# Kernel optimization log

Measured on AMD Instinct MI355X. Metric: run time of the kernel, lower is better.

## Reference

```python
import jax, jax.numpy as jnp
import numpy as np

D = 256
H_GRID = 256
W_GRID = 256
N_LAYERS = 6


def _build_edges(H, W):
    # Vectorized equivalent of grid_to_graph's 4-neighbor edge construction.
    ii, jj = np.meshgrid(np.arange(H), np.arange(W), indexing='ij')
    srcs, dsts, feats = [], [], []
    for di, dj in [(-1, 0), (1, 0), (0, -1), (0, 1)]:
        ni, nj = ii + di, jj + dj
        m = (ni >= 0) & (ni < H) & (nj >= 0) & (nj < W)
        s = (ii * W + jj)[m]
        d = (ni * W + nj)[m]
        f = np.stack([
            np.full(s.shape, di, np.float32),
            np.full(s.shape, dj, np.float32),
            (ii[m] / H).astype(np.float32),
            (jj[m] / W).astype(np.float32),
        ], axis=-1)
        srcs.append(s); dsts.append(d); feats.append(f)
    edge_index = np.stack([np.concatenate(srcs), np.concatenate(dsts)]).astype(np.int32)
    edge_feats = np.concatenate(feats).astype(np.float32)
    return edge_index, edge_feats


def setup_inputs() -> dict:
    key = jax.random.key(0)
    ks = jax.random.split(key, 16)
    grid = jax.random.randint(ks[0], (H_GRID, W_GRID), 0, 10, dtype=jnp.int32)
    edge_index_np, edge_feats_np = _build_edges(H_GRID, W_GRID)
    edge_index = jnp.asarray(edge_index_np)
    edge_feats = jnp.asarray(edge_feats_np)

    def lin(k, fan_in, fan_out):
        bound = 1.0 / np.sqrt(fan_in)
        k1, k2 = jax.random.split(k)
        W = jax.random.uniform(k1, (fan_in, fan_out), jnp.float32, -bound, bound)
        b = jax.random.uniform(k2, (fan_out,), jnp.float32, -bound, bound)
        return W, b

    node_W, node_b = lin(ks[1], 1, D)

    def stack_lin(k, fan_in, fan_out):
        keys = jax.random.split(k, N_LAYERS)
        Ws, bs = zip(*[lin(kk, fan_in, fan_out) for kk in keys])
        return jnp.stack(Ws), jnp.stack(bs)

    msg_W1, msg_b1 = stack_lin(ks[2], 2 * D + 4, D)
    msg_W2, msg_b2 = stack_lin(ks[3], D, D)
    upd_W1, upd_b1 = stack_lin(ks[4], 2 * D, D)
    upd_W2, upd_b2 = stack_lin(ks[5], D, D)
    out_W, out_b = lin(ks[6], D, 10)

    return {
        'grid': grid, 'edge_index': edge_index, 'edge_feats': edge_feats,
        'node_W': node_W, 'node_b': node_b,
        'msg_W1': msg_W1, 'msg_b1': msg_b1, 'msg_W2': msg_W2, 'msg_b2': msg_b2,
        'upd_W1': upd_W1, 'upd_b1': upd_b1, 'upd_W2': upd_W2, 'upd_b2': upd_b2,
        'out_W': out_W, 'out_b': out_b,
    }


def reference(grid, edge_index, edge_feats, node_W, node_b,
              msg_W1, msg_b1, msg_W2, msg_b2,
              upd_W1, upd_b1, upd_W2, upd_b2,
              out_W, out_b):
    H, W = grid.shape
    N = H * W
    nodes = grid.astype(jnp.float32).reshape(N, 1)         # [N,1]
    h = nodes @ node_W + node_b                              # [N,D]
    src, tgt = edge_index[0], edge_index[1]

    def layer(h, params):
        mW1, mb1, mW2, mb2, uW1, ub1, uW2, ub2 = params
        # gather per-edge source/target features, run message MLP
        msg_in = jnp.concatenate([h[src], h[tgt], edge_feats], axis=-1)  # [E,2D+4]
        m = jax.nn.relu(msg_in @ mW1 + mb1) @ mW2 + mb2                   # [E,D]
        # scatter-add messages onto target nodes (vectorized segment sum)
        agg = jax.ops.segment_sum(m, tgt, num_segments=N)                 # [N,D]
        u_in = jnp.concatenate([h, agg], axis=-1)                         # [N,2D]
        h_new = jax.nn.relu(u_in @ uW1 + ub1) @ uW2 + ub2                 # [N,D]
        return h_new, None

    h, _ = jax.lax.scan(layer, h, (msg_W1, msg_b1, msg_W2, msg_b2,
                                   upd_W1, upd_b1, upd_W2, upd_b2))
    out = h @ out_W + out_b                                  # [N,10]
    return out.reshape(H, W, 10)
```

## Files before the change

### kernel.cpp

```cpp
#include <hip/hip_runtime.h>

#define HG 256
#define WGD 256
#define NN (HG*WGD)
#define NL 6

typedef _Float16 f16;
typedef _Float16 f16x8 __attribute__((ext_vector_type(8)));
typedef float f32x4 __attribute__((ext_vector_type(4)));

__device__ __forceinline__ void gload_lds16(const f16* g, f16* lds) {
  __builtin_amdgcn_global_load_lds(
      (const __attribute__((address_space(1))) unsigned int*)g,
      (__attribute__((address_space(3))) unsigned int*)lds, 16, 0, 0);
}

template<int KK, int EPI>
__global__ __launch_bounds__(512) void gemm8(
    const f16* __restrict__ A, int lda,
    const f16* __restrict__ Bt, int ldb,
    f16* __restrict__ C, int ldc,
    const float* __restrict__ bias,
    const float* __restrict__ v2,
    const float* __restrict__ avec,
    const int* __restrict__ gridv)
{
  constexpr int NT = KK/64;
  __shared__ f16 As[2][128*64];
  __shared__ f16 Bs[2][256*64];
  const int tid  = threadIdx.x;
  const int lane = tid & 63;
  const int w    = tid >> 6;
  const int wm   = w >> 2, wn = w & 3;

  int bid = blockIdx.x * gridDim.y + blockIdx.y;
  const int nwg = gridDim.x * gridDim.y;
  { int q = nwg >> 3; bid = (bid & 7) * q + (bid >> 3); }
  const int by = bid % gridDim.y, bx = bid / gridDim.y;
  const int mbase = bx * 128;
  const int nbase = by * 256;

  f32x4 acc[4][4];
#pragma unroll
  for (int a=0;a<4;a++)
#pragma unroll
    for (int b=0;b<4;b++) acc[a][b] = (f32x4){0.f,0.f,0.f,0.f};

  const int r8  = lane >> 3;
  const int c8s = ((lane & 7) ^ r8) * 8;

#define STAGE8(kt, buf)                                                        \
  {                                                                            \
    const f16* Ab = A + (size_t)mbase*lda + (kt)*64;                           \
    _Pragma("unroll")                                                          \
    for (int p=0;p<2;p++) {                                                    \
      int qc = p*8 + w;                                                        \
      gload_lds16(Ab + (size_t)(qc*8 + r8)*lda + c8s, &As[buf][qc*512]);       \
    }                                                                          \
    const f16* Bb = Bt + (size_t)nbase*ldb + (kt)*64;                          \
    _Pragma("unroll")                                                          \
    for (int p=0;p<4;p++) {                                                    \
      int qc = p*8 + w;                                                        \
      gload_lds16(Bb + (size_t)(qc*8 + r8)*ldb + c8s, &Bs[buf][qc*512]);       \
    }                                                                          \
  }

  STAGE8(0, 0);
  __syncthreads();
  int cur = 0;
  for (int kt = 0; kt < NT; ++kt) {
    if (kt + 1 < NT) STAGE8(kt + 1, cur ^ 1);
    const f16* Acur = &As[cur][0];
    const f16* Bcur = &Bs[cur][0];
#pragma unroll
    for (int ks=0; ks<2; ++ks) {
      const int off = (((ks*4 + (lane>>4)) ^ (lane & 7)) * 8);
      f16x8 af[4], bf[4];
#pragma unroll
      for (int fm=0; fm<4; ++fm)
        af[fm] = *(const f16x8*)&Acur[(wm*64 + fm*16 + (lane&15))*64 + off];
#pragma unroll
      for (int fn=0; fn<4; ++fn)
        bf[fn] = *(const f16x8*)&Bcur[(wn*64 + fn*16 + (lane&15))*64 + off];
#pragma unroll
      for (int fm=0; fm<4; ++fm)
#pragma unroll
        for (int fn=0; fn<4; ++fn)
          acc[fm][fn] = __builtin_amdgcn_mfma_f32_16x16x32_f16(af[fm], bf[fn], acc[fm][fn], 0,0,0);
    }
    __syncthreads();
    cur ^= 1;
  }
#undef STAGE8

  const int row0 = mbase + wm*64 + (lane>>4)*4;
  const int col0 = nbase + wn*64 + (lane&15);
#pragma unroll
  for (int fm=0; fm<4; ++fm) {
#pragma unroll
    for (int fn=0; fn<4; ++fn) {
      const int col = col0 + fn*16;
#pragma unroll
      for (int r=0;r<4;r++) {
        int row = row0 + fm*16 + r;
        float v = acc[fm][fn][r];
        if (EPI==1 || EPI==3) {
          int i = row >> 8, j = row & 255;
          float deg = (float)((i>0)+(i<255)+(j>0)+(j<255));
          v += bias[col & 255] + deg * v2[col & 255];
          if (EPI==3) v += (float)gridv[row] * avec[col & 255];
          v = fmaxf(v, 0.f);
        } else if (EPI==2) {
          v += bias[col];
        }
        C[(size_t)row*ldc + col] = (f16)v;
      }
    }
  }
}

__device__ __forceinline__ void gemm_core256(
    const f16* __restrict__ A, int lda,
    const f16* __restrict__ Bt, int ldb,
    f16* __restrict__ C, int ldc,
    int mbase, int nbase, f16* As, f16* Bs)
{
  const int tid  = threadIdx.x;
  const int lane = tid & 63;
  const int w    = tid >> 6;
  const int wm   = w >> 1, wn = w & 1;

  f32x4 acc[4][4];
#pragma unroll
  for (int a=0;a<4;a++)
#pragma unroll
    for (int b=0;b<4;b++) acc[a][b] = (f32x4){0.f,0.f,0.f,0.f};

  const int r8  = lane >> 3;
  const int c8s = ((lane & 7) ^ r8) * 8;

  for (int kt = 0; kt < 4; ++kt) {
    const f16* Ab = A  + (size_t)(mbase + w*32)*lda + kt*64;
    const f16* Bb = Bt + (size_t)(nbase + w*32)*ldb + kt*64;
#pragma unroll
    for (int i=0;i<4;i++) {
      gload_lds16(Ab + (size_t)(i*8 + r8)*lda + c8s, &As[(w*32+i*8)*64]);
      gload_lds16(Bb + (size_t)(i*8 + r8)*ldb + c8s, &Bs[(w*32+i*8)*64]);
    }
    __syncthreads();
#pragma unroll
    for (int ks=0; ks<2; ++ks) {
      const int off = (((ks*4 + (lane>>4)) ^ (lane & 7)) * 8);
      f16x8 af[4], bf[4];
#pragma unroll
      for (int fm=0; fm<4; ++fm)
        af[fm] = *(const f16x8*)&As[(wm*64 + fm*16 + (lane&15))*64 + off];
#pragma unroll
      for (int fn=0; fn<4; ++fn)
        bf[fn] = *(const f16x8*)&Bs[(wn*64 + fn*16 + (lane&15))*64 + off];
#pragma unroll
      for (int fm=0; fm<4; ++fm)
#pragma unroll
        for (int fn=0; fn<4; ++fn)
          acc[fm][fn] = __builtin_amdgcn_mfma_f32_16x16x32_f16(af[fm], bf[fn], acc[fm][fn], 0,0,0);
    }
    __syncthreads();
  }

  const int row0 = mbase + wm*64 + (lane>>4)*4;
  const int col0 = nbase + wn*64 + (lane&15);
#pragma unroll
  for (int fm=0; fm<4; ++fm)
#pragma unroll
    for (int fn=0; fn<4; ++fn)
#pragma unroll
      for (int r=0;r<4;r++)
        C[(size_t)(row0 + fm*16 + r)*ldc + (col0 + fn*16)] = (f16)acc[fm][fn][r];
}

__global__ __launch_bounds__(256) void fold_all(
    const f16* __restrict__ BtA,  const f16* __restrict__ uW2h,
    const f16* __restrict__ mW2h, const f16* __restrict__ uW1aT,
    const f16* __restrict__ uW1bT,const f16* __restrict__ oWTh,
    f16* __restrict__ BtPQ, f16* __restrict__ BtU, f16* __restrict__ Wp2t)
{
  __shared__ f16 As[128*64];
  __shared__ f16 Bs[128*64];
  const int b = blockIdx.x;
  if (b < 40) {
    int z = b >> 3, rem = b & 7, x = rem & 3, y = rem >> 2;
    gemm_core256(BtA + (size_t)(z+1)*131072, 256, uW2h + (size_t)z*65536, 256,
                 BtPQ + (size_t)(z+1)*131072, 256, x*128, y*128, As, Bs);
  } else if (b < 60) {
    int rem = b - 40, z = rem >> 2, r2 = rem & 3, x = r2 & 1, y = r2 >> 1;
    gemm_core256(uW1aT + (size_t)(z+1)*65536, 256, uW2h + (size_t)z*65536, 256,
                 BtU + (size_t)(z+1)*131072, 512, x*128, y*128, As, Bs);
  } else if (b < 84) {
    int rem = b - 60, z = rem >> 2, r2 = rem & 3, x = r2 & 1, y = r2 >> 1;
    gemm_core256(uW1bT + (size_t)z*65536, 256, mW2h + (size_t)z*65536, 256,
                 BtU + (size_t)z*131072 + 256, 512, x*128, y*128, As, Bs);
  } else {
    int y = b - 84;
    gemm_core256(oWTh, 256, uW2h + (size_t)5*65536, 256,
                 Wp2t, 256, 0, y*128, As, Bs);
  }
}

template<int R1>
__global__ __launch_bounds__(256) void edge_fuse(
    const f16* __restrict__ PQ, f16* __restrict__ UR,
    const float* __restrict__ cvec, const float* __restrict__ wsi_,
    const float* __restrict__ wsj_,
    const int* __restrict__ gridv, const float* __restrict__ pa,
    const float* __restrict__ pc)
{
  const int t  = threadIdx.x;
  const int ln = t >> 5, ch = t & 31;
  int bid = blockIdx.x;
  bid = (bid & 7) * 1024 + (bid >> 3);
  const int n  = bid*8 + ln;
  const int i  = n >> 8, j = n & 255;
  const int co = ch*8;

  float q[8], pa0[8], pc0[8];
  if (R1) {
    float g = (float)gridv[n];
#pragma unroll
    for (int e=0;e<8;e++) {
      pa0[e] = pa[co+e]; pc0[e] = pc[co+e];
      q[e] = g*pa[256+co+e] + pc[256+co+e];
    }
  } else {
    f16x8 qv = *(const f16x8*)&PQ[(size_t)n*512 + 256 + co];
#pragma unroll
    for (int e=0;e<8;e++) q[e] = (float)qv[e];
  }
  float wi[8], wj[8];
#pragma unroll
  for (int e=0;e<8;e++){ wi[e]=wsi_[co+e]; wj[e]=wsj_[co+e]; }
  float acc[8];
#pragma unroll
  for (int e=0;e<8;e++) acc[e]=0.f;

  const int DI[4] = {-1,1,0,0};
  const int DJ[4] = {0,0,-1,1};
#pragma unroll
  for (int d=0; d<4; ++d) {
    int si = i - DI[d], sj = j - DJ[d];
    if (si>=0 && si<HG && sj>=0 && sj<WGD) {
      int s = si*WGD + sj;
      float fsi = si * (1.f/HG), fsj = sj * (1.f/WGD);
      float pvf[8];
      if (R1) {
        float gs = (float)gridv[s];
#pragma unroll
        for (int e=0;e<8;e++) pvf[e] = gs*pa0[e] + pc0[e];
      } else {
        f16x8 pv = *(const f16x8*)&PQ[(size_t)s*512 + co];
#pragma unroll
        for (int e=0;e<8;e++) pvf[e] = (float)pv[e];
      }
#pragma unroll
      for (int e=0;e<8;e++) {
        float v = pvf[e] + q[e] + cvec[d*256+co+e] + fsi*wi[e] + fsj*wj[e];
        acc[e] += fmaxf(v, 0.f);
      }
    }
  }
  f16x8 outv;
#pragma unroll
  for (int e=0;e<8;e++) outv[e] = (f16)acc[e];
  *(f16x8*)&UR[(size_t)n*512 + 256 + co] = outv;
}

__global__ __launch_bounds__(256) void out_mfma(
    const f16* __restrict__ U,
    const f16* __restrict__ Wp2t,
    const float* __restrict__ ob2,
    float* __restrict__ out)
{
  int lane = threadIdx.x & 63;
  int wv   = threadIdx.x >> 6;
  int nbase = blockIdx.x*64 + wv*16;
  f32x4 acc = (f32x4){0.f,0.f,0.f,0.f};
  int r  = lane & 15;
  int kg = (lane >> 4) * 8;
  const f16* Up = U + (size_t)(nbase + r)*512 + kg;
  const f16* Bp = Wp2t + r*256 + kg;
#pragma unroll
  for (int kt=0; kt<8; ++kt) {
    f16x8 af = *(const f16x8*)(Up + kt*32);
    f16x8 bf = *(const f16x8*)(Bp + kt*32);
    acc = __builtin_amdgcn_mfma_f32_16x16x32_f16(af, bf, acc, 0,0,0);
  }
  int col = lane & 15;
  int row0 = (lane>>4)*4;
  if (col < 10) {
    float bo = ob2[col];
#pragma unroll
    for (int rr=0; rr<4; ++rr)
      out[(size_t)(nbase + row0 + rr)*10 + col] = acc[rr] + bo;
  }
}

__global__ __launch_bounds__(256) void prep_small(
    const float* __restrict__ uW2, const float* __restrict__ mW2,
    const float* __restrict__ oW,  const float* __restrict__ mW1,
    const float* __restrict__ mb1, const float* __restrict__ mb2,
    const float* __restrict__ uW1, const float* __restrict__ ub1,
    const float* __restrict__ ub2, const float* __restrict__ nb,
    const float* __restrict__ nW,  const float* __restrict__ ob,
    f16* __restrict__ uW2h, f16* __restrict__ mW2h, f16* __restrict__ oWTh,
    float* __restrict__ cvec, float* __restrict__ wsi_, float* __restrict__ wsj_,
    float* __restrict__ v2, float* __restrict__ ubias, float* __restrict__ avec,
    float* __restrict__ pqb, float* __restrict__ pa, float* __restrict__ pc,
    float* __restrict__ ob2,
    f16* __restrict__ BtA, f16* __restrict__ uW1aT, f16* __restrict__ uW1bT)
{
  __shared__ float red[3][4][64];
  __shared__ float tbuf[32][33];
  const int b = blockIdx.x;
  const int tid = threadIdx.x;
  if (b < 1536) {
    int idx = b*256 + tid;
    uW2h[idx] = (f16)uW2[idx];
    mW2h[idx] = (f16)mW2[idx];
  } else if (b < 1664) {
    int c = b - 1536, j = tid;
    oWTh[c*256 + j] = (c < 10) ? (f16)oW[j*10 + c] : (f16)0.f;
  } else if (b < 1670) {
    int l = b - 1664, j = tid;
    const float* base = mW1 + (size_t)l*516*256;
    float w512 = base[512*256 + j], w513 = base[513*256 + j];
    float b1 = mb1[l*256 + j];
    const int DI[4] = {-1,1,0,0};
    const int DJ[4] = {0,0,-1,1};
    for (int d=0;d<4;d++)
      cvec[(l*4+d)*256 + j] = (float)DI[d]*w512 + (float)DJ[d]*w513 + b1;
    wsi_[l*256+j] = base[514*256 + j];
    wsj_[l*256+j] = base[515*256 + j];
  } else if (b < 1694) {
    int pr = tid & 63, q = tid >> 6;
    int pair = (b-1670)*64 + pr;
    int l = pair >> 8, j = pair & 255;
    const float* prevb = l ? (ub2 + (l-1)*256) : nb;
    float s1=0.f, s2=0.f, s3=0.f;
    for (int t = q*64; t < q*64+64; ++t) {
      s1 += mb2[l*256+t] * uW1[((size_t)l*512+256+t)*256 + j];
      s2 += prevb[t]     * uW1[((size_t)l*512+t)*256 + j];
      if (l==0) s3 += nW[t] * uW1[(size_t)t*256 + j];
    }
    red[0][q][pr]=s1; red[1][q][pr]=s2; red[2][q][pr]=s3;
    __syncthreads();
    if (q==0) {
      float a = red[0][0][pr]+red[0][1][pr]+red[0][2][pr]+red[0][3][pr];
      float bb = red[1][0][pr]+red[1][1][pr]+red[1][2][pr]+red[1][3][pr];
      v2[pair] = a;
      ubias[pair] = ub1[pair] + bb;
      if (l==0) avec[j] = red[2][0][pr]+red[2][1][pr]+red[2][2][pr]+red[2][3][pr];
    }
  } else if (b < 1742) {
    int pr = tid & 63, q = tid >> 6;
    int pair = (b-1694)*64 + pr;
    int l = pair >> 9, c = pair & 511;
    int rowoff = (c < 256) ? 0 : 256;
    int cc = c & 255;
    const float* base = mW1 + (size_t)l*516*256 + (size_t)rowoff*256 + cc;
    float s1=0.f, s2=0.f;
    if (l==0) {
      for (int j=q*64; j<q*64+64; ++j) { float wv = base[(size_t)j*256]; s1 += nW[j]*wv; s2 += nb[j]*wv; }
    } else {
      const float* pb = ub2 + (l-1)*256;
      for (int j=q*64; j<q*64+64; ++j) s1 += pb[j]*base[(size_t)j*256];
    }
    red[0][q][pr]=s1; red[1][q][pr]=s2;
    __syncthreads();
    if (q==0) {
      float a = red[0][0][pr]+red[0][1][pr]+red[0][2][pr]+red[0][3][pr];
      if (l==0) { pa[c]=a; pc[c]=red[1][0][pr]+red[1][1][pr]+red[1][2][pr]+red[1][3][pr]; }
      else pqb[pair] = a;
    }
  } else if (b == 1742) {
    int c = tid >> 4, jg = tid & 15;
    float s = 0.f;
    if (c < 10)
      for (int j=jg*16; j<jg*16+16; ++j) s += ub2[5*256+j]*oW[j*10+c];
    red[0][c>>2][(c&3)*16+jg] = s;
    __syncthreads();
    if (jg==0 && c < 16) {
      float a=0.f;
      for (int t2=0;t2<16;t2++) a += red[0][c>>2][(c&3)*16+t2];
      ob2[c] = (c < 10) ? a + ob[c] : 0.f;
    }
  } else {
    int t = b - 1743;
    int z = t >> 6, rem = t & 63;
    int bxs = (rem & 7) * 32, bys = (rem >> 3) * 32;
    const int q = z / 6, l = z % 6;
    const float* s;
    f16* d;
    if (q == 0)      { s = mW1 + (size_t)l*516*256;          d = BtA   + (size_t)l*131072; }
    else if (q == 1) { s = mW1 + (size_t)l*516*256 + 65536;  d = BtA   + (size_t)l*131072 + 65536; }
    else if (q == 2) { s = uW1 + (size_t)l*131072;           d = uW1aT + (size_t)l*65536; }
    else             { s = uW1 + (size_t)l*131072 + 65536;   d = uW1bT + (size_t)l*65536; }
    const int tx = tid & 31, ty = tid >> 5;
#pragma unroll
    for (int rr=0; rr<4; ++rr)
      tbuf[ty+rr*8][tx] = s[(size_t)(bys+ty+rr*8)*256 + bxs+tx];
    __syncthreads();
#pragma unroll
    for (int rr=0; rr<4; ++rr)
      d[(size_t)(bxs+ty+rr*8)*256 + bys+tx] = (f16)tbuf[tx][ty+rr*8];
  }
}

extern "C" void kernel_launch(void* const* d_in, const int* in_sizes, int n_in,
                              void* d_out, int out_size, void* d_ws, size_t ws_size,
                              hipStream_t stream)
{
  const int*   gridv = (const int*) d_in[0];
  const float* nW   = (const float*)d_in[3];
  const float* nb   = (const float*)d_in[4];
  const float* mW1  = (const float*)d_in[5];
  const float* mb1  = (const float*)d_in[6];
  const float* mW2  = (const float*)d_in[7];
  const float* mb2  = (const float*)d_in[8];
  const float* uW1  = (const float*)d_in[9];
  const float* ub1  = (const float*)d_in[10];
  const float* uW2  = (const float*)d_in[11];
  const float* ub2  = (const float*)d_in[12];
  const float* oW   = (const float*)d_in[13];
  const float* ob   = (const float*)d_in[14];
  float* out = (float*)d_out;

  char* ws = (char*)d_ws;
  size_t off = 0;
  f16* URa  = (f16*)(ws + off); off += (size_t)NN*512*2;
  f16* URb  = (f16*)(ws + off); off += (size_t)NN*512*2;
  f16* BtA  = (f16*)(ws + off); off += 6*512*256*2;
  f16* BtPQ = (f16*)(ws + off); off += 6*512*256*2;
  f16* BtU  = (f16*)(ws + off); off += 6*256*512*2;
  f16* uW2h = (f16*)(ws + off); off += 6*256*256*2;
  f16* mW2h = (f16*)(ws + off); off += 6*256*256*2;
  f16* uW1aT= (f16*)(ws + off); off += 6*256*256*2;
  f16* uW1bT= (f16*)(ws + off); off += 6*256*256*2;
  f16* oWTh = (f16*)(ws + off); off += 128*256*2;
  f16* Wp2t = (f16*)(ws + off); off += 128*256*2;
  float* cvec = (float*)(ws + off); off += 6*4*256*4;
  float* wsi_ = (float*)(ws + off); off += 6*256*4;
  float* wsj_ = (float*)(ws + off); off += 6*256*4;
  float* v2   = (float*)(ws + off); off += 6*256*4;
  float* ubias= (float*)(ws + off); off += 6*256*4;
  float* pqb  = (float*)(ws + off); off += 6*512*4;
  float* pa   = (float*)(ws + off); off += 512*4;
  float* pc   = (float*)(ws + off); off += 512*4;
  float* avec = (float*)(ws + off); off += 256*4;
  float* ob2  = (float*)(ws + off); off += 16*4;

  prep_small<<<3279,256,0,stream>>>(uW2, mW2, oW, mW1, mb1, mb2, uW1, ub1, ub2,
                                    nb, nW, ob,
                                    uW2h, mW2h, oWTh, cvec, wsi_, wsj_,
                                    v2, ubias, avec, pqb, pa, pc, ob2,
                                    BtA, uW1aT, uW1bT);
  fold_all<<<86,256,0,stream>>>(BtA, uW2h, mW2h, uW1aT, uW1bT, oWTh,
                                BtPQ, BtU, Wp2t);

  edge_fuse<1><<<8192,256,0,stream>>>(nullptr, URa, cvec, wsi_, wsj_, gridv, pa, pc);
  gemm8<256,3><<<dim3(512,1),512,0,stream>>>(
      URa + 256, 512, BtU + 256, 512, URa, 512,
      ubias, v2, avec, gridv);

  f16* cur = URa; f16* nxt = URb;
  for (int l=1;l<NL;l++){
    gemm8<256,2><<<dim3(512,2),512,0,stream>>>(
        cur, 512, BtPQ + (size_t)l*131072, 256, nxt, 512,
        pqb + l*512, nullptr, nullptr, nullptr);
    edge_fuse<0><<<8192,256,0,stream>>>(nxt, cur, cvec + l*1024, wsi_ + l*256, wsj_ + l*256,
                                        nullptr, nullptr, nullptr);
    gemm8<512,1><<<dim3(512,1),512,0,stream>>>(
        cur, 512, BtU + (size_t)l*131072, 512, nxt, 512,
        ubias + l*256, v2 + l*256, nullptr, nullptr);
    f16* t = cur; cur = nxt; nxt = t;
  }

  out_mfma<<<1024,256,0,stream>>>(cur, Wp2t, ob2, out);
}
```

Before: 522.5 us.

## Fuse update GEMM with next layer's PQ projection GEMM per row tile

Adds a gemm_merge kernel that computes the update MLP output for a 128-row tile, stages the fp16 result in LDS, then immediately multiplies it by the next layer's PQ projection weights. This removes one kernel launch per layer and the global round-trip that re-read h to compute PQ. It needs an extra NN x 512 PQ buffer. The layer loop is restructured so the last layer still uses the plain gemm8.

```diff
diff --git a/kernel.cpp b/kernel.cpp
--- a/kernel.cpp
+++ b/kernel.cpp
@@ -114,6 +114,163 @@
           v += bias[col];
         }
         C[(size_t)row*ldc + col] = (f16)v;
+      }
+    }
+  }
+}
+
+template<int KK, int EPI>
+__global__ __launch_bounds__(512) void gemm_merge(
+    const f16* __restrict__ A, int lda,
+    const f16* __restrict__ BtU_,
+    const f16* __restrict__ BtPQ_,
+    f16* __restrict__ Uo,
+    f16* __restrict__ PQo,
+    const float* __restrict__ bias,
+    const float* __restrict__ v2,
+    const float* __restrict__ avec,
+    const int* __restrict__ gridv,
+    const float* __restrict__ bias2)
+{
+  constexpr int NT = KK/64;
+  __shared__ f16 As[2][128*64];
+  __shared__ f16 Bs[2][256*64];
+  const int tid  = threadIdx.x;
+  const int lane = tid & 63;
+  const int w    = tid >> 6;
+  const int wm   = w >> 2, wn = w & 3;
+
+  int bid = blockIdx.x;
+  bid = (bid & 7) * 64 + (bid >> 3);
+  const int mbase = bid * 128;
+
+  f32x4 acc[4][4];
+#pragma unroll
+  for (int a=0;a<4;a++)
+#pragma unroll
+    for (int b=0;b<4;b++) acc[a][b] = (f32x4){0.f,0.f,0.f,0.f};
+
+  const int r8  = lane >> 3;
+  const int c8s = ((lane & 7) ^ r8) * 8;
+
+#define STAGEM(kt, buf)                                                        \
+  {                                                                            \
+    const f16* Ab = A + (size_t)mbase*lda + (kt)*64;                           \
+    _Pragma("unroll")                                                          \
+    for (int p=0;p<2;p++) {                                                    \
+      int qc = p*8 + w;                                                        \
+      gload_lds16(Ab + (size_t)(qc*8 + r8)*lda + c8s, &As[buf][qc*512]);       \
+    }                                                                          \
+    const f16* Bb = BtU_ + (kt)*64;                                            \
+    _Pragma("unroll")                                                          \
+    for (int p=0;p<4;p++) {                                                    \
+      int qc = p*8 + w;                                                        \
+      gload_lds16(Bb + (size_t)(qc*8 + r8)*512 + c8s, &Bs[buf][qc*512]);       \
+    }                                                                          \
+  }
+
+  STAGEM(0, 0);
+  __syncthreads();
+  int cur = 0;
+  for (int kt = 0; kt < NT; ++kt) {
+    if (kt + 1 < NT) STAGEM(kt + 1, cur ^ 1);
+    const f16* Acur = &As[cur][0];
+    const f16* Bcur = &Bs[cur][0];
+#pragma unroll
+    for (int ks=0; ks<2; ++ks) {
+      const int off = (((ks*4 + (lane>>4)) ^ (lane & 7)) * 8);
+      f16x8 af[4], bf[4];
+#pragma unroll
+      for (int fm=0; fm<4; ++fm)
+        af[fm] = *(const f16x8*)&Acur[(wm*64 + fm*16 + (lane&15))*64 + off];
+#pragma unroll
+      for (int fn=0; fn<4; ++fn)
+        bf[fn] = *(const f16x8*)&Bcur[(wn*64 + fn*16 + (lane&15))*64 + off];
+#pragma unroll
+      for (int fm=0; fm<4; ++fm)
+#pragma unroll
+        for (int fn=0; fn<4; ++fn)
+          acc[fm][fn] = __builtin_amdgcn_mfma_f32_16x16x32_f16(af[fm], bf[fn], acc[fm][fn], 0,0,0);
+    }
+    __syncthreads();
+    cur ^= 1;
+  }
+#undef STAGEM
+
+  f16* Ul = &Bs[0][0];
+#pragma unroll
+  for (int fm=0; fm<4; ++fm) {
+#pragma unroll
+    for (int fn=0; fn<4; ++fn) {
+      const int coll = wn*64 + fn*16 + (lane&15);
+#pragma unroll
+      for (int r=0;r<4;r++) {
+        int rl  = wm*64 + (lane>>4)*4 + fm*16 + r;
+        int row = mbase + rl;
+        float v = acc[fm][fn][r];
+        int i = row >> 8, j = row & 255;
+        float deg = (float)((i>0)+(i<255)+(j>0)+(j<255));
+        v += bias[coll] + deg * v2[coll];
+        if (EPI==3) v += (float)gridv[row] * avec[coll];
+        v = fmaxf(v, 0.f);
+        f16 hv = (f16)v;
+        Uo[(size_t)row*512 + coll] = hv;
+        int sblk = (coll >> 3) ^ (rl & 7);
+        Ul[rl*256 + sblk*8 + (coll & 7)] = hv;
+      }
+    }
+  }
+  __syncthreads();
+
+  f16* Bc = &As[0][0];
+  for (int h=0; h<2; ++h) {
+    f32x4 acc2[4][4];
+#pragma unroll
+    for (int a=0;a<4;a++)
+#pragma unroll
+      for (int b=0;b<4;b++) acc2[a][b] = (f32x4){0.f,0.f,0.f,0.f};
+    for (int kt=0; kt<4; ++kt) {
+      const f16* Bb = BtPQ_ + (size_t)(h*256)*256 + kt*64;
+#pragma unroll
+      for (int p=0;p<4;p++) {
+        int qc = p*8 + w;
+        gload_lds16(Bb + (size_t)(qc*8 + r8)*256 + c8s, &Bc[qc*512]);
+      }
+      __syncthreads();
+#pragma unroll
+      for (int ks=0; ks<2; ++ks) {
+        f16x8 af[4], bf[4];
+#pragma unroll
+        for (int fm=0; fm<4; ++fm) {
+          int rl = wm*64 + fm*16 + (lane&15);
+          int sblk = (kt*8 + ks*4 + (lane>>4)) ^ (rl & 7);
+          af[fm] = *(const f16x8*)&Ul[rl*256 + sblk*8];
+        }
+#pragma unroll
+        for (int fn=0; fn<4; ++fn) {
+          int rb = wn*64 + fn*16 + (lane&15);
+          int off = (((ks*4 + (lane>>4)) ^ (rb & 7)) * 8);
+          bf[fn] = *(const f16x8*)&Bc[rb*64 + off];
+        }
+#pragma unroll
+        for (int fm=0; fm<4; ++fm)
+#pragma unroll
+          for (int fn=0; fn<4; ++fn)
+            acc2[fm][fn] = __builtin_amdgcn_mfma_f32_16x16x32_f16(af[fm], bf[fn], acc2[fm][fn], 0,0,0);
+      }
+      __syncthreads();
+    }
+    const float* b2 = bias2 + h*256;
+#pragma unroll
+    for (int fm=0; fm<4; ++fm) {
+#pragma unroll
+      for (int fn=0; fn<4; ++fn) {
+        const int coll = wn*64 + fn*16 + (lane&15);
+#pragma unroll
+        for (int r=0;r<4;r++) {
+          int row = mbase + wm*64 + (lane>>4)*4 + fm*16 + r;
+          PQo[(size_t)row*512 + h*256 + coll] = (f16)(acc2[fm][fn][r] + b2[coll]);
+        }
       }
     }
   }
@@ -437,6 +594,7 @@
   size_t off = 0;
   f16* URa  = (f16*)(ws + off); off += (size_t)NN*512*2;
   f16* URb  = (f16*)(ws + off); off += (size_t)NN*512*2;
+  f16* PQ   = (f16*)(ws + off); off += (size_t)NN*512*2;
   f16* BtA  = (f16*)(ws + off); off += 6*512*256*2;
   f16* BtPQ = (f16*)(ws + off); off += 6*512*256*2;
   f16* BtU  = (f16*)(ws + off); off += 6*256*512*2;
@@ -466,22 +624,25 @@
                                 BtPQ, BtU, Wp2t);
 
   edge_fuse<1><<<8192,256,0,stream>>>(nullptr, URa, cvec, wsi_, wsj_, gridv, pa, pc);
-  gemm8<256,3><<<dim3(512,1),512,0,stream>>>(
-      URa + 256, 512, BtU + 256, 512, URa, 512,
-      ubias, v2, avec, gridv);
-
-  f16* cur = URa; f16* nxt = URb;
-  for (int l=1;l<NL;l++){
-    gemm8<256,2><<<dim3(512,2),512,0,stream>>>(
-        cur, 512, BtPQ + (size_t)l*131072, 256, nxt, 512,
-        pqb + l*512, nullptr, nullptr, nullptr);
-    edge_fuse<0><<<8192,256,0,stream>>>(nxt, cur, cvec + l*1024, wsi_ + l*256, wsj_ + l*256,
+  gemm_merge<256,3><<<512,512,0,stream>>>(
+      URa + 256, 512, BtU + 256, BtPQ + (size_t)1*131072,
+      URb, PQ, ubias, v2, avec, gridv, pqb + 1*512);
+
+  f16* cur = URb; f16* nxt = URa;
+  for (int l=1;l<5;l++){
+    edge_fuse<0><<<8192,256,0,stream>>>(PQ, cur, cvec + l*1024, wsi_ + l*256, wsj_ + l*256,
                                         nullptr, nullptr, nullptr);
-    gemm8<512,1><<<dim3(512,1),512,0,stream>>>(
-        cur, 512, BtU + (size_t)l*131072, 512, nxt, 512,
-        ubias + l*256, v2 + l*256, nullptr, nullptr);
+    gemm_merge<512,1><<<512,512,0,stream>>>(
+        cur, 512, BtU + (size_t)l*131072, BtPQ + (size_t)(l+1)*131072,
+        nxt, PQ, ubias + l*256, v2 + l*256, nullptr, nullptr, pqb + (l+1)*512);
     f16* t = cur; cur = nxt; nxt = t;
   }
 
-  out_mfma<<<1024,256,0,stream>>>(cur, Wp2t, ob2, out);
-}
+  edge_fuse<0><<<8192,256,0,stream>>>(PQ, cur, cvec + 5*1024, wsi_ + 5*256, wsj_ + 5*256,
+                                      nullptr, nullptr, nullptr);
+  gemm8<512,1><<<dim3(512,1),512,0,stream>>>(
+      cur, 512, BtU + (size_t)5*131072, 512, nxt, 512,
+      ubias + 5*256, v2 + 5*256, nullptr, nullptr);
+
+  out_mfma<<<1024,256,0,stream>>>(nxt, Wp2t, ob2, out);
+}
```

Result: faster. 486.8 us (-6.8%).

## Fuse per-layer PQ projection GEMM into the update GEMM epilogue

Applied to the files above, without the earlier changes.

The update GEMM now uses 64-row tiles covering all 256 output columns. It keeps its relu output tile in LDS and immediately multiplies it by the next layer's PQ weights, writing PQ into a separate buffer. This removes the standalone PQ GEMM launch and one full re-read of the node features per layer. In exchange there is a smaller per-block tile with less reuse of B, more LDS use, an extra workspace buffer, and a reworked ping-pong schedule.

```diff
diff --git a/kernel.cpp b/kernel.cpp
--- a/kernel.cpp
+++ b/kernel.cpp
@@ -15,108 +15,166 @@
       (__attribute__((address_space(3))) unsigned int*)lds, 16, 0, 0);
 }
 
-template<int KK, int EPI>
-__global__ __launch_bounds__(512) void gemm8(
+template<int KK, int EPI, int DOPQ>
+__global__ __launch_bounds__(512,4) void gemm_merge(
     const f16* __restrict__ A, int lda,
-    const f16* __restrict__ Bt, int ldb,
-    f16* __restrict__ C, int ldc,
+    const f16* __restrict__ BtU_,
+    const f16* __restrict__ BtPQ_,
+    f16* __restrict__ Uo,
+    f16* __restrict__ PQo,
     const float* __restrict__ bias,
     const float* __restrict__ v2,
     const float* __restrict__ avec,
-    const int* __restrict__ gridv)
+    const int* __restrict__ gridv,
+    const float* __restrict__ bias2)
 {
   constexpr int NT = KK/64;
-  __shared__ f16 As[2][128*64];
-  __shared__ f16 Bs[2][256*64];
+  __shared__ f16 sh[40960];
   const int tid  = threadIdx.x;
   const int lane = tid & 63;
   const int w    = tid >> 6;
-  const int wm   = w >> 2, wn = w & 3;
-
-  int bid = blockIdx.x * gridDim.y + blockIdx.y;
-  const int nwg = gridDim.x * gridDim.y;
-  { int q = nwg >> 3; bid = (bid & 7) * q + (bid >> 3); }
-  const int by = bid % gridDim.y, bx = bid / gridDim.y;
-  const int mbase = bx * 128;
-  const int nbase = by * 256;
-
-  f32x4 acc[4][4];
+
+  int bid = blockIdx.x;
+  bid = (bid & 7) * 128 + (bid >> 3);
+  const int mbase = bid * 64;
+
+  f32x4 acc[4][2];
 #pragma unroll
   for (int a=0;a<4;a++)
 #pragma unroll
-    for (int b=0;b<4;b++) acc[a][b] = (f32x4){0.f,0.f,0.f,0.f};
+    for (int b=0;b<2;b++) acc[a][b] = (f32x4){0.f,0.f,0.f,0.f};
 
   const int r8  = lane >> 3;
   const int c8s = ((lane & 7) ^ r8) * 8;
 
-#define STAGE8(kt, buf)                                                        \
+#define ASB(b) (sh + (b)*4096)
+#define BSB(b) (sh + 8192 + (b)*16384)
+#define UL (sh)
+#define BC (sh + 16384)
+
+#define STAGEM(kt, buf)                                                        \
   {                                                                            \
-    const f16* Ab = A + (size_t)mbase*lda + (kt)*64;                           \
-    _Pragma("unroll")                                                          \
-    for (int p=0;p<2;p++) {                                                    \
-      int qc = p*8 + w;                                                        \
-      gload_lds16(Ab + (size_t)(qc*8 + r8)*lda + c8s, &As[buf][qc*512]);       \
-    }                                                                          \
-    const f16* Bb = Bt + (size_t)nbase*ldb + (kt)*64;                          \
+    gload_lds16(A + (size_t)(mbase + w*8 + r8)*lda + (kt)*64 + c8s,            \
+                ASB(buf) + w*512);                                             \
+    const f16* Bb = BtU_ + (kt)*64;                                            \
     _Pragma("unroll")                                                          \
     for (int p=0;p<4;p++) {                                                    \
       int qc = p*8 + w;                                                        \
-      gload_lds16(Bb + (size_t)(qc*8 + r8)*ldb + c8s, &Bs[buf][qc*512]);       \
+      gload_lds16(Bb + (size_t)(qc*8 + r8)*512 + c8s, BSB(buf) + qc*512);      \
     }                                                                          \
   }
 
-  STAGE8(0, 0);
+  STAGEM(0, 0);
   __syncthreads();
   int cur = 0;
   for (int kt = 0; kt < NT; ++kt) {
-    if (kt + 1 < NT) STAGE8(kt + 1, cur ^ 1);
-    const f16* Acur = &As[cur][0];
-    const f16* Bcur = &Bs[cur][0];
+    if (kt + 1 < NT) STAGEM(kt + 1, cur ^ 1);
+    const f16* Acur = ASB(cur);
+    const f16* Bcur = BSB(cur);
 #pragma unroll
     for (int ks=0; ks<2; ++ks) {
       const int off = (((ks*4 + (lane>>4)) ^ (lane & 7)) * 8);
-      f16x8 af[4], bf[4];
+      f16x8 af[4], bf[2];
 #pragma unroll
       for (int fm=0; fm<4; ++fm)
-        af[fm] = *(const f16x8*)&Acur[(wm*64 + fm*16 + (lane&15))*64 + off];
-#pragma unroll
-      for (int fn=0; fn<4; ++fn)
-        bf[fn] = *(const f16x8*)&Bcur[(wn*64 + fn*16 + (lane&15))*64 + off];
+        af[fm] = *(const f16x8*)&Acur[(fm*16 + (lane&15))*64 + off];
+#pragma unroll
+      for (int fn=0; fn<2; ++fn)
+        bf[fn] = *(const f16x8*)&Bcur[(w*32 + fn*16 + (lane&15))*64 + off];
 #pragma unroll
       for (int fm=0; fm<4; ++fm)
 #pragma unroll
-        for (int fn=0; fn<4; ++fn)
+        for (int fn=0; fn<2; ++fn)
           acc[fm][fn] = __builtin_amdgcn_mfma_f32_16x16x32_f16(af[fm], bf[fn], acc[fm][fn], 0,0,0);
     }
     __syncthreads();
     cur ^= 1;
   }
-#undef STAGE8
-
-  const int row0 = mbase + wm*64 + (lane>>4)*4;
-  const int col0 = nbase + wn*64 + (lane&15);
+#undef STAGEM
+
 #pragma unroll
   for (int fm=0; fm<4; ++fm) {
 #pragma unroll
-    for (int fn=0; fn<4; ++fn) {
-      const int col = col0 + fn*16;
+    for (int fn=0; fn<2; ++fn) {
+      const int coll = w*32 + fn*16 + (lane&15);
 #pragma unroll
       for (int r=0;r<4;r++) {
-        int row = row0 + fm*16 + r;
+        int rl  = fm*16 + (lane>>4)*4 + r;
+        int row = mbase + rl;
         float v = acc[fm][fn][r];
-        if (EPI==1 || EPI==3) {
-          int i = row >> 8, j = row & 255;
-          float deg = (float)((i>0)+(i<255)+(j>0)+(j<255));
-          v += bias[col & 255] + deg * v2[col & 255];
-          if (EPI==3) v += (float)gridv[row] * avec[col & 255];
-          v = fmaxf(v, 0.f);
-        } else if (EPI==2) {
-          v += bias[col];
+        int i = row >> 8, j = row & 255;
+        float deg = (float)((i>0)+(i<255)+(j>0)+(j<255));
+        v += bias[coll] + deg * v2[coll];
+        if (EPI==3) v += (float)gridv[row] * avec[coll];
+        v = fmaxf(v, 0.f);
+        f16 hv = (f16)v;
+        Uo[(size_t)row*512 + coll] = hv;
+        if (DOPQ) {
+          int sblk = (coll >> 3) ^ (rl & 7);
+          UL[rl*256 + sblk*8 + (coll & 7)] = hv;
         }
-        C[(size_t)row*ldc + col] = (f16)v;
       }
     }
   }
+
+  if (DOPQ) {
+    __syncthreads();
+    for (int h=0; h<2; ++h) {
+      f32x4 acc2[4][2];
+#pragma unroll
+      for (int a=0;a<4;a++)
+#pragma unroll
+        for (int b=0;b<2;b++) acc2[a][b] = (f32x4){0.f,0.f,0.f,0.f};
+      for (int kt=0; kt<4; ++kt) {
+        const f16* Bb = BtPQ_ + (size_t)(h*256)*256 + kt*64;
+#pragma unroll
+        for (int p=0;p<4;p++) {
+          int qc = p*8 + w;
+          gload_lds16(Bb + (size_t)(qc*8 + r8)*256 + c8s, BC + qc*512);
+        }
+        __syncthreads();
+#pragma unroll
+        for (int ks=0; ks<2; ++ks) {
+          f16x8 af[4], bf[2];
+#pragma unroll
+          for (int fm=0; fm<4; ++fm) {
+            int rl = fm*16 + (lane&15);
+            int sblk = (kt*8 + ks*4 + (lane>>4)) ^ (rl & 7);
+            af[fm] = *(const f16x8*)&UL[rl*256 + sblk*8];
+          }
+#pragma unroll
+          for (int fn=0; fn<2; ++fn) {
+            int rb = w*32 + fn*16 + (lane&15);
+            int offb = (((ks*4 + (lane>>4)) ^ (rb & 7)) * 8);
+            bf[fn] = *(const f16x8*)&BC[rb*64 + offb];
+          }
+#pragma unroll
+          for (int fm=0; fm<4; ++fm)
+#pragma unroll
+            for (int fn=0; fn<2; ++fn)
+              acc2[fm][fn] = __builtin_amdgcn_mfma_f32_16x16x32_f16(af[fm], bf[fn], acc2[fm][fn], 0,0,0);
+        }
+        __syncthreads();
+      }
+      const float* b2 = bias2 + h*256;
+#pragma unroll
+      for (int fm=0; fm<4; ++fm) {
+#pragma unroll
+        for (int fn=0; fn<2; ++fn) {
+          const int coll = w*32 + fn*16 + (lane&15);
+#pragma unroll
+          for (int r=0;r<4;r++) {
+            int row = mbase + fm*16 + (lane>>4)*4 + r;
+            PQo[(size_t)row*512 + h*256 + coll] = (f16)(acc2[fm][fn][r] + b2[coll]);
+          }
+        }
+      }
+    }
+  }
+#undef ASB
+#undef BSB
+#undef UL
+#undef BC
 }
 
 __device__ __forceinline__ void gemm_core256(
@@ -437,6 +495,7 @@
   size_t off = 0;
   f16* URa  = (f16*)(ws + off); off += (size_t)NN*512*2;
   f16* URb  = (f16*)(ws + off); off += (size_t)NN*512*2;
+  f16* PQ   = (f16*)(ws + off); off += (size_t)NN*512*2;
   f16* BtA  = (f16*)(ws + off); off += 6*512*256*2;
   f16* BtPQ = (f16*)(ws + off); off += 6*512*256*2;
   f16* BtU  = (f16*)(ws + off); off += 6*256*512*2;
@@ -466,22 +525,25 @@
                                 BtPQ, BtU, Wp2t);
 
   edge_fuse<1><<<8192,256,0,stream>>>(nullptr, URa, cvec, wsi_, wsj_, gridv, pa, pc);
-  gemm8<256,3><<<dim3(512,1),512,0,stream>>>(
-      URa + 256, 512, BtU + 256, 512, URa, 512,
-      ubias, v2, avec, gridv);
-
-  f16* cur = URa; f16* nxt = URb;
-  for (int l=1;l<NL;l++){
-    gemm8<256,2><<<dim3(512,2),512,0,stream>>>(
-        cur, 512, BtPQ + (size_t)l*131072, 256, nxt, 512,
-        pqb + l*512, nullptr, nullptr, nullptr);
-    edge_fuse<0><<<8192,256,0,stream>>>(nxt, cur, cvec + l*1024, wsi_ + l*256, wsj_ + l*256,
+  gemm_merge<256,3,1><<<1024,512,0,stream>>>(
+      URa + 256, 512, BtU + 256, BtPQ + (size_t)1*131072,
+      URb, PQ, ubias, v2, avec, gridv, pqb + 1*512);
+
+  f16* cur = URb; f16* nxt = URa;
+  for (int l=1;l<5;l++){
+    edge_fuse<0><<<8192,256,0,stream>>>(PQ, cur, cvec + l*1024, wsi_ + l*256, wsj_ + l*256,
                                         nullptr, nullptr, nullptr);
-    gemm8<512,1><<<dim3(512,1),512,0,stream>>>(
-        cur, 512, BtU + (size_t)l*131072, 512, nxt, 512,
-        ubias + l*256, v2 + l*256, nullptr, nullptr);
+    gemm_merge<512,1,1><<<1024,512,0,stream>>>(
+        cur, 512, BtU + (size_t)l*131072, BtPQ + (size_t)(l+1)*131072,
+        nxt, PQ, ubias + l*256, v2 + l*256, nullptr, nullptr, pqb + (l+1)*512);
     f16* t = cur; cur = nxt; nxt = t;
   }
 
-  out_mfma<<<1024,256,0,stream>>>(cur, Wp2t, ob2, out);
-}
+  edge_fuse<0><<<8192,256,0,stream>>>(PQ, cur, cvec + 5*1024, wsi_ + 5*256, wsj_ + 5*256,
+                                      nullptr, nullptr, nullptr);
+  gemm_merge<512,1,0><<<1024,512,0,stream>>>(
+      cur, 512, BtU + (size_t)5*131072, nullptr,
+      nxt, nullptr, ubias + 5*256, v2 + 5*256, nullptr, nullptr, nullptr);
+
+  out_mfma<<<1024,256,0,stream>>>(nxt, Wp2t, ob2, out);
+}
```

Measured after the change: 449.9 us. 13.9% less time.
